# Optimization experiments

Measured on AMD Instinct MI355X. Metric: run time of the kernel, lower is better.

Reference implementation:

```python
import jax, jax.numpy as jnp
import numpy as np

B, S, H = 2, 1024, 4096
NH, NKV, D = 32, 8, 128
EPS = 1e-6
THETA = 10000.0


def rotate_half(x):
    x1, x2 = jnp.split(x, 2, axis=-1)
    return jnp.concatenate([-x2, x1], axis=-1)


def rmsnorm(x, w, eps):
    # RMSNorm over the last (head_dim) axis
    var = jnp.mean(x * x, axis=-1, keepdims=True)
    return x * jax.lax.rsqrt(var + eps) * w


def setup_inputs() -> dict:
    key = jax.random.key(0)
    ks = jax.random.split(key, 6)
    hidden_states = jax.random.normal(ks[0], (B, S, H), dtype=jnp.float32)
    # scaled init so activations stay O(1)
    Wq = jax.random.normal(ks[1], (NH * D, H), dtype=jnp.float32) * (H ** -0.5)
    Wk = jax.random.normal(ks[2], (NKV * D, H), dtype=jnp.float32) * (H ** -0.5)
    Wv = jax.random.normal(ks[3], (NKV * D, H), dtype=jnp.float32) * (H ** -0.5)
    Wo = jax.random.normal(ks[4], (H, NH * D), dtype=jnp.float32) * ((NH * D) ** -0.5)
    q_norm_w = jnp.ones((D,), dtype=jnp.float32)
    k_norm_w = jnp.ones((D,), dtype=jnp.float32)
    # standard default RoPE cos/sin tables, broadcast to [B, S, D]
    pos = jnp.arange(S, dtype=jnp.float32)
    inv_freq = 1.0 / (THETA ** (jnp.arange(0, D, 2, dtype=jnp.float32) / D))
    freqs = pos[:, None] * inv_freq[None, :]            # [S, D/2]
    emb = jnp.concatenate([freqs, freqs], axis=-1)      # [S, D]
    cos = jnp.broadcast_to(jnp.cos(emb)[None], (B, S, D)).astype(jnp.float32)
    sin = jnp.broadcast_to(jnp.sin(emb)[None], (B, S, D)).astype(jnp.float32)
    return dict(hidden_states=hidden_states, cos=cos, sin=sin,
                Wq=Wq, Wk=Wk, Wv=Wv, Wo=Wo,
                q_norm_w=q_norm_w, k_norm_w=k_norm_w)


def reference(hidden_states, cos, sin, Wq, Wk, Wv, Wo, q_norm_w, k_norm_w):
    b, s, h = hidden_states.shape
    # fused QKV projections (MojoLinear: y = x @ W.T, no bias)
    q = (hidden_states @ Wq.T).reshape(b, s, NH, D)
    k = (hidden_states @ Wk.T).reshape(b, s, NKV, D)
    v = (hidden_states @ Wv.T).reshape(b, s, NKV, D)
    # per-head-dim RMSNorm on q and k, then [B, H, S, D] layout
    q = rmsnorm(q, q_norm_w, EPS).transpose(0, 2, 1, 3)   # [B, NH,  S, D]
    k = rmsnorm(k, k_norm_w, EPS).transpose(0, 2, 1, 3)   # [B, NKV, S, D]
    v = v.transpose(0, 2, 1, 3)                           # [B, NKV, S, D]
    # RoPE (rotate-half)
    c = cos[:, None, :, :]
    sn = sin[:, None, :, :]
    q = q * c + rotate_half(q) * sn
    k = k * c + rotate_half(k) * sn
    # GQA: expand KV heads to query heads
    groups = NH // NKV
    k = jnp.repeat(k, groups, axis=1)                     # [B, NH, S, D]
    v = jnp.repeat(v, groups, axis=1)
    # causal attention (prefill with empty paged cache == causal SDPA)
    scores = jnp.einsum('bhqd,bhkd->bhqk', q, k) * (D ** -0.5)
    causal = jnp.tril(jnp.ones((s, s), dtype=bool))
    scores = jnp.where(causal, scores, jnp.finfo(scores.dtype).min)
    probs = jax.nn.softmax(scores, axis=-1)
    out = jnp.einsum('bhqk,bhkd->bhqd', probs, v)         # [B, NH, S, D]
    out = out.transpose(0, 2, 1, 3).reshape(b, s, NH * D)
    return out @ Wo.T
```

## Files before the change

kernel.cpp:

```cpp
#include <hip/hip_runtime.h>


typedef float  f32x4   __attribute__((ext_vector_type(4)));
typedef float  f32x16  __attribute__((ext_vector_type(16)));
typedef __bf16 bf16x8  __attribute__((ext_vector_type(8)));
typedef unsigned short u16x8 __attribute__((ext_vector_type(8)));

__device__ __forceinline__ unsigned short f2b(float f) {
    union { float f; unsigned int u; } x;
    x.f = f;
    unsigned int u = x.u;
    unsigned int r = u + 0x7fffu + ((u >> 16) & 1u);
    return (unsigned short)(r >> 16);
}

__device__ __forceinline__ void async16(const unsigned short* g, unsigned short* l) {
    __builtin_amdgcn_global_load_lds(
        (const __attribute__((address_space(1))) void*)g,
        (__attribute__((address_space(3))) void*)l, 16, 0, 0);
}

__global__ __launch_bounds__(256) void cvt_all(const float* __restrict__ hsrc,
                                               const float* __restrict__ wq,
                                               const float* __restrict__ wk,
                                               const float* __restrict__ wv,
                                               const float* __restrict__ wo,
                                               unsigned short* __restrict__ hidb,
                                               unsigned short* __restrict__ wqkvb,
                                               unsigned short* __restrict__ wob) {
    int i = blockIdx.x * 256 + threadIdx.x;
    if (i >= 6291456) return;
    const float* s; unsigned short* d; int j;
    if (i < 1048576)      { s = hsrc; d = hidb;             j = i; }
    else if (i < 3145728) { s = wq;   d = wqkvb;            j = i - 1048576; }
    else if (i < 3670016) { s = wk;   d = wqkvb + 16777216; j = i - 3145728; }
    else if (i < 4194304) { s = wv;   d = wqkvb + 20971520; j = i - 3670016; }
    else                  { s = wo;   d = wob;              j = i - 4194304; }
    const float4* s4 = (const float4*)s + (size_t)j * 2;
    float4 a = s4[0], b = s4[1];
    u16x8 o;
    o[0] = f2b(a.x); o[1] = f2b(a.y); o[2] = f2b(a.z); o[3] = f2b(a.w);
    o[4] = f2b(b.x); o[5] = f2b(b.y); o[6] = f2b(b.z); o[7] = f2b(b.w);
    *((u16x8*)d + j) = o;
}

__global__ __launch_bounds__(512, 2) void gemm256_bt(const unsigned short* __restrict__ A,
                                                     const unsigned short* __restrict__ W,
                                                     float* __restrict__ C) {
    constexpr int K = 4096, N = 6144;
    __shared__ __align__(16) unsigned short Ab[3][256 * 64];
    __shared__ __align__(16) unsigned short Bb[2][192 * 64];

    const int tid  = threadIdx.x;
    const int wave = tid >> 6, lane = tid & 63;
    const int wm   = wave >> 2, wn = wave & 3;
    const int l15  = lane & 15, h = lane >> 4;
    const int cx0  = (h ^ (l15 & 7)) << 3;
    const int cx1  = cx0 ^ 32;
    const int stgrow = wave * 8 + (lane >> 3);
    const int stgcol = ((lane & 7) ^ (lane >> 3)) << 3;
    const int aRow0 = blockIdx.y * 256;
    const int bRow0 = blockIdx.x * 192;
    const int NT = K >> 6;

#define STAGE_A(t, s, bi) async16(A + (size_t)(aRow0 + (s)*64 + stgrow) * K + (t)*64 + stgcol, \
                                  &Ab[bi][(s)*4096 + wave*512])
#define STAGE_B(t, s, bi) async16(W + (size_t)(bRow0 + (s)*64 + stgrow) * K + (t)*64 + stgcol, \
                                  &Bb[bi][(s)*4096 + wave*512])
#define RD_AQ(dst, buf, q) do { \
    _Pragma("unroll") \
    for (int mi = 0; mi < 2; mi++) { \
        const unsigned short* ap_ = (buf) + (wm * 128 + (q) * 32 + mi * 16 + l15) * 64; \
        dst[mi][0] = *(const bf16x8*)(ap_ + cx0); \
        dst[mi][1] = *(const bf16x8*)(ap_ + cx1); \
    } } while (0)
#define RD_B(dst, buf) do { \
    _Pragma("unroll") \
    for (int nf = 0; nf < 3; nf++) { \
        const unsigned short* bp_ = (buf) + (wn * 48 + nf * 16 + l15) * 64; \
        dst[nf][0] = *(const bf16x8*)(bp_ + cx0); \
        dst[nf][1] = *(const bf16x8*)(bp_ + cx1); \
    } } while (0)
#define MFMA_Q(q, AR, BR) do { \
    _Pragma("unroll") \
    for (int mi = 0; mi < 2; mi++) \
    _Pragma("unroll") \
    for (int nf = 0; nf < 3; nf++) { \
        acc[(q)*2+mi][nf] = __builtin_amdgcn_mfma_f32_16x16x32_bf16(AR[mi][0], BR[nf][0], acc[(q)*2+mi][nf], 0, 0, 0); \
        acc[(q)*2+mi][nf] = __builtin_amdgcn_mfma_f32_16x16x32_bf16(AR[mi][1], BR[nf][1], acc[(q)*2+mi][nf], 0, 0, 0); \
    } } while (0)
#define SB()      __builtin_amdgcn_sched_barrier(0)
#define BARRIER() __builtin_amdgcn_s_barrier()
#define PRIO1()   __builtin_amdgcn_s_setprio(1)
#define PRIO0()   __builtin_amdgcn_s_setprio(0)
#define LGKM(n)   asm volatile("s_waitcnt lgkmcnt(" #n ")" ::: "memory")

#define TILE(T, BC, BN_) do { \
    const int t_ = (T); \
    const unsigned short* Ab_ = Ab[t_ % 3]; \
    const int rb1 = (t_ & 1) ^ 1, ra2 = (t_ + 2) % 3; \
    const bool sb = (t_ + 1 < NT), sa = (t_ + 2 < NT); \
     \
    RD_AQ(rB, Ab_, 1); \
    if (sb) { STAGE_B(t_ + 1, 0, rb1); STAGE_B(t_ + 1, 1, rb1); STAGE_B(t_ + 1, 2, rb1); } \
    SB(); LGKM(4); SB(); \
    PRIO1(); MFMA_Q(0, rA, BC); PRIO0(); SB(); \
     \
    RD_AQ(rC, Ab_, 2); \
    if (sa) { STAGE_A(t_ + 2, 0, ra2); STAGE_A(t_ + 2, 1, ra2); } \
    SB(); LGKM(4); SB(); \
    PRIO1(); MFMA_Q(1, rB, BC); PRIO0(); SB(); \
     \
    RD_AQ(rD, Ab_, 3); \
    if (sa) { STAGE_A(t_ + 2, 2, ra2); STAGE_A(t_ + 2, 3, ra2); } \
    SB(); LGKM(4); SB(); \
    PRIO1(); MFMA_Q(2, rC, BC); PRIO0(); SB(); \
     \
    if (sa) asm volatile("s_waitcnt vmcnt(4)" ::: "memory"); \
    else    asm volatile("s_waitcnt vmcnt(0)" ::: "memory"); \
    SB(); BARRIER(); SB(); \
    if (sb) { RD_B(BN_, Bb[(t_ + 1) & 1]); RD_AQ(rA, Ab[(t_ + 1) % 3], 0); } \
    SB(); \
    if (sb) { LGKM(10); } else { LGKM(0); } \
    SB(); \
    PRIO1(); MFMA_Q(3, rD, BC); PRIO0(); SB(); \
} while (0)

    f32x4 acc[8][3] = {};
    bf16x8 rA[2][2], rB[2][2], rC[2][2], rD[2][2];
    bf16x8 bc[3][2], bn[3][2];

    STAGE_B(0, 0, 0); STAGE_B(0, 1, 0); STAGE_B(0, 2, 0);
    STAGE_A(0, 0, 0); STAGE_A(0, 1, 0); STAGE_A(0, 2, 0); STAGE_A(0, 3, 0);
    STAGE_A(1, 0, 1); STAGE_A(1, 1, 1); STAGE_A(1, 2, 1); STAGE_A(1, 3, 1);
    asm volatile("s_waitcnt vmcnt(4)" ::: "memory");
    SB(); BARRIER(); SB();
    RD_B(bc, Bb[0]);
    RD_AQ(rA, Ab[0], 0);
    SB();

    for (int t = 0; t < NT; t += 2) {
        TILE(t,     bc, bn);
        TILE(t + 1, bn, bc);
    }

    #pragma unroll
    for (int mf = 0; mf < 8; mf++)
        #pragma unroll
        for (int nf = 0; nf < 3; nf++)
            #pragma unroll
            for (int r = 0; r < 4; r++) {
                int row = aRow0 + wm * 128 + mf * 16 + h * 4 + r;
                int col = bRow0 + wn * 48 + nf * 16 + l15;
                C[(size_t)row * N + col] = acc[mf][nf][r];
            }
#undef STAGE_A
#undef STAGE_B
#undef RD_AQ
#undef RD_B
#undef MFMA_Q
#undef SB
#undef BARRIER
#undef PRIO1
#undef PRIO0
#undef LGKM
#undef TILE
}

__global__ __launch_bounds__(256) void gemm_bt_bf16(const unsigned short* __restrict__ A,
                                                    const unsigned short* __restrict__ W,
                                                    float* __restrict__ C,
                                                    int K, int N) {
    __shared__ __align__(16) unsigned short As[128 * 64];
    __shared__ __align__(16) unsigned short Bs[128 * 64];

    const int tid  = threadIdx.x;
    const int wave = tid >> 6, lane = tid & 63;
    const int wm   = wave >> 1, wn = wave & 1;
    const int l31  = lane & 31, lh = lane >> 5;
    const int arow = blockIdx.y * 128, brow = blockIdx.x * 128;

    int rr[4], gc[4], slot[4];
    #pragma unroll
    for (int it = 0; it < 4; it++) {
        slot[it] = it * 4 + wave;
        int ci = slot[it] * 64 + lane;
        rr[it] = ci >> 3;
        int c  = ci & 7;
        gc[it] = c ^ (rr[it] & 7);
    }

    f32x16 acc[2][2] = {};

    for (int k0 = 0; k0 < K; k0 += 64) {
        #pragma unroll
        for (int it = 0; it < 4; it++) {
            async16(A + (size_t)(arow + rr[it]) * K + k0 + gc[it] * 8, &As[slot[it] * 512]);
            async16(W + (size_t)(brow + rr[it]) * K + k0 + gc[it] * 8, &Bs[slot[it] * 512]);
        }
        __syncthreads();

        bf16x8 af[4][2], bfr[4][2];
        #pragma unroll
        for (int ks = 0; ks < 4; ks++) {
            #pragma unroll
            for (int i = 0; i < 2; i++) {
                int rowa = wm * 64 + i * 32 + l31;
                int ch   = (ks * 2 + lh) ^ (rowa & 7);
                af[ks][i]  = *(const bf16x8*)&As[rowa * 64 + ch * 8];
                int rowb = wn * 64 + i * 32 + l31;
                int chb  = (ks * 2 + lh) ^ (rowb & 7);
                bfr[ks][i] = *(const bf16x8*)&Bs[rowb * 64 + chb * 8];
            }
        }
        #pragma unroll
        for (int ks = 0; ks < 4; ks++)
            #pragma unroll
            for (int i = 0; i < 2; i++)
                #pragma unroll
                for (int j = 0; j < 2; j++)
                    acc[i][j] = __builtin_amdgcn_mfma_f32_32x32x16_bf16(af[ks][i], bfr[ks][j], acc[i][j], 0, 0, 0);
        __syncthreads();
    }

    #pragma unroll
    for (int i = 0; i < 2; i++)
        #pragma unroll
        for (int j = 0; j < 2; j++)
            #pragma unroll
            for (int r = 0; r < 16; r++) {
                int row = arow + wm * 64 + i * 32 + lh * 4 + (r & 3) + 8 * (r >> 2);
                int col = brow + wn * 64 + j * 32 + l31;
                C[(size_t)row * N + col] = acc[i][j][r];
            }
}

__global__ __launch_bounds__(256) void norm_rope(const float* __restrict__ X, int rstride,
                                                 const float* __restrict__ cosp,
                                                 const float* __restrict__ sinp,
                                                 const float* __restrict__ w,
                                                 unsigned short* __restrict__ Y, int nh) {
    const int wid  = blockIdx.x * 4 + (threadIdx.x >> 6);
    const int lane = threadIdx.x & 63;
    const int row  = wid / nh;
    const int h    = wid - row * nh;

    const float* xp = X + (size_t)row * rstride + h * 128;
    float x0 = xp[lane], x1 = xp[lane + 64];
    float ss = x0 * x0 + x1 * x1;
    #pragma unroll
    for (int off = 32; off; off >>= 1) ss += __shfl_xor(ss, off, 64);
    float r = rsqrtf(ss * (1.0f / 128.0f) + 1e-6f);
    float n0 = x0 * r * w[lane];
    float n1 = x1 * r * w[lane + 64];
    const float* cp = cosp + (size_t)row * 128;
    const float* sp = sinp + (size_t)row * 128;
    float y0 = n0 * cp[lane]      - n1 * sp[lane];
    float y1 = n1 * cp[lane + 64] + n0 * sp[lane + 64];
    const int b = row >> 10, s = row & 1023;
    unsigned short* yp = Y + (((size_t)(b * nh + h)) * 1024 + s) * 128;
    yp[lane]      = f2b(y0);
    yp[lane + 64] = f2b(y1);
}

__global__ __launch_bounds__(256) void v_trans(const float* __restrict__ V,
                                               unsigned short* __restrict__ Vt) {
    __shared__ float T[64][65];
    const int tid = threadIdx.x;
    const int st = blockIdx.x >> 1, dt = blockIdx.x & 1;
    const int bh = blockIdx.y, b = bh >> 3, h = bh & 7;

    const int sl = tid >> 2, c0 = (tid & 3) * 16;
    const float* src = V + (size_t)(b * 1024 + st * 64 + sl) * 6144 + h * 128 + dt * 64 + c0;
    #pragma unroll
    for (int j = 0; j < 4; j++) {
        float4 v = *(const float4*)(src + j * 4);
        *(float4*)&T[sl][c0 + j * 4] = v;
    }
    __syncthreads();

    const int dgrp = tid >> 6, sl2 = tid & 63;
    unsigned short* dst = Vt + (size_t)bh * 131072 + st * 64 + sl2;
    #pragma unroll
    for (int jd = 0; jd < 16; jd++) {
        int dl = dgrp * 16 + jd;
        dst[(size_t)(dt * 64 + dl) * 1024] = f2b(T[sl2][dl]);
    }
}

__global__ __launch_bounds__(256) void attn(const unsigned short* __restrict__ Qb,
                                            const unsigned short* __restrict__ Kb,
                                            const unsigned short* __restrict__ Vt,
                                            unsigned short* __restrict__ Ob) {
    __shared__ __align__(16) unsigned short Klds[128 * 128];
    __shared__ __align__(16) unsigned short Plds[4][16][136];

    const int tid  = threadIdx.x;
    const int w    = tid >> 6, lane = tid & 63;
    const int quad = lane >> 4, l15 = lane & 15;
    const int h = blockIdx.y, b = blockIdx.z, kvh = h >> 2;

    const unsigned short* Qp = Qb + ((size_t)(b * 32 + h))   * 131072;
    const unsigned short* Kp = Kb + ((size_t)(b * 8 + kvh))  * 131072;
    const unsigned short* Vp = Vt + ((size_t)(b * 8 + kvh))  * 131072;
    const float c2 = (float)(0.08838834764831845 * 1.4426950408889634);

    for (int half = 0; half < 2; half++) {
        const int qt = half ? (15 - (int)blockIdx.x) : (int)blockIdx.x;
        const int q0 = qt * 64;
        const int qrow = q0 + w * 16 + l15;

        bf16x8 qf[4];
        #pragma unroll
        for (int ks = 0; ks < 4; ks++)
            qf[ks] = *(const bf16x8*)(Qp + (size_t)qrow * 128 + ks * 32 + quad * 8);

        float m_i[4], l_i[4];
        #pragma unroll
        for (int r = 0; r < 4; r++) { m_i[r] = -1e30f; l_i[r] = 0.0f; }
        f32x4 o[8] = {};

        const int ntiles = (qt >> 1) + 1;
        const int nfull  = (qt * 64 + 1) >> 7;

        for (int kt = 0; kt < ntiles; kt++) {
            __syncthreads();
            #pragma unroll
            for (int it = 0; it < 8; it++) {
                int slot = it * 4 + w;
                int ci = slot * 64 + lane;
                int r = ci >> 4, c = ci & 15;
                int g = (c & 8) | ((c ^ r) & 7);
                async16(Kp + (size_t)(kt * 128 + r) * 128 + g * 8, &Klds[slot * 512]);
            }
            __syncthreads();

            f32x4 sacc[8] = {};
            __builtin_amdgcn_s_setprio(1);
            #pragma unroll
            for (int ks = 0; ks < 4; ks++) {
                #pragma unroll
                for (int tn = 0; tn < 8; tn++) {
                    int row = tn * 16 + l15;
                    int ch  = ks * 4 + quad;
                    int chs = (ch & 8) | ((ch ^ row) & 7);
                    bf16x8 kf = *(const bf16x8*)&Klds[row * 128 + chs * 8];
                    sacc[tn] = __builtin_amdgcn_mfma_f32_16x16x32_bf16(qf[ks], kf, sacc[tn], 0, 0, 0);
                }
            }
            __builtin_amdgcn_s_setprio(0);

            const bool masked = (kt >= nfull);
            #pragma unroll
            for (int r = 0; r < 4; r++) {
                float sv[8];
                float rmax = -1e30f;
                if (masked) {
                    const int qg = q0 + w * 16 + quad * 4 + r;
                    #pragma unroll
                    for (int tn = 0; tn < 8; tn++) {
                        float v = sacc[tn][r];
                        int kg = kt * 128 + tn * 16 + l15;
                        if (kg > qg) v = -1e30f;
                        sv[tn] = v;
                        rmax = fmaxf(rmax, v);
                    }
                } else {
                    #pragma unroll
                    for (int tn = 0; tn < 8; tn++) {
                        sv[tn] = sacc[tn][r];
                        rmax = fmaxf(rmax, sv[tn]);
                    }
                }
                #pragma unroll
                for (int off = 8; off; off >>= 1) rmax = fmaxf(rmax, __shfl_xor(rmax, off, 16));
                float mnew  = fmaxf(m_i[r], rmax);
                float alpha = __builtin_amdgcn_exp2f((m_i[r] - mnew) * c2);
                float rsum  = 0.0f;
                #pragma unroll
                for (int tn = 0; tn < 8; tn++) {
                    float p = __builtin_amdgcn_exp2f((sv[tn] - mnew) * c2);
                    sv[tn] = p;
                    rsum += p;
                }
                #pragma unroll
                for (int off = 8; off; off >>= 1) rsum += __shfl_xor(rsum, off, 16);
                m_i[r] = mnew;
                l_i[r] = l_i[r] * alpha + rsum;
                #pragma unroll
                for (int td = 0; td < 8; td++) o[td][r] *= alpha;
                #pragma unroll
                for (int tn = 0; tn < 8; tn++)
                    Plds[w][quad * 4 + r][tn * 16 + l15] = f2b(sv[tn]);
            }

            __builtin_amdgcn_s_setprio(1);
            #pragma unroll
            for (int ks = 0; ks < 4; ks++) {
                bf16x8 pf = *(const bf16x8*)&Plds[w][l15][ks * 32 + quad * 8];
                #pragma unroll
                for (int td = 0; td < 8; td++) {
                    bf16x8 vf = *(const bf16x8*)(Vp + (size_t)(td * 16 + l15) * 1024 + kt * 128 + ks * 32 + quad * 8);
                    o[td] = __builtin_amdgcn_mfma_f32_16x16x32_bf16(pf, vf, o[td], 0, 0, 0);
                }
            }
            __builtin_amdgcn_s_setprio(0);
        }

        #pragma unroll
        for (int r = 0; r < 4; r++) {
            float inv = 1.0f / l_i[r];
            const int qg = q0 + w * 16 + quad * 4 + r;
            unsigned short* op = Ob + ((size_t)(b * 1024 + qg)) * 4096 + h * 128;
            #pragma unroll
            for (int td = 0; td < 8; td++)
                op[td * 16 + l15] = f2b(o[td][r] * inv);
        }
    }
}

extern "C" void kernel_launch(void* const* d_in, const int* in_sizes, int n_in,
                              void* d_out, int out_size, void* d_ws, size_t ws_size,
                              hipStream_t stream) {
    const float* hid  = (const float*)d_in[0];
    const float* cosp = (const float*)d_in[1];
    const float* sinp = (const float*)d_in[2];
    const float* Wq   = (const float*)d_in[3];
    const float* Wk   = (const float*)d_in[4];
    const float* Wv   = (const float*)d_in[5];
    const float* Wo   = (const float*)d_in[6];
    const float* qw   = (const float*)d_in[7];
    const float* kw   = (const float*)d_in[8];
    float* out = (float*)d_out;

    char* ws = (char*)d_ws;
    float* QKVf = (float*)ws;
    unsigned short* Ob = (unsigned short*)ws;
    size_t off = (size_t)2048 * 6144 * 4;
    unsigned short* hidb  = (unsigned short*)(ws + off); off += (size_t)2048 * 4096 * 2;
    unsigned short* Wqkvb = (unsigned short*)(ws + off); off += (size_t)6144 * 4096 * 2;
    unsigned short* Wob   = (unsigned short*)(ws + off);
    unsigned short* Qb    = hidb;
    unsigned short* Kb    = Wqkvb;
    unsigned short* Vt    = Wqkvb + (size_t)2048 * 1024;

    dim3 blk(256);
    cvt_all<<<24576, blk, 0, stream>>>(hid, Wq, Wk, Wv, Wo, hidb, Wqkvb, Wob);
    gemm256_bt<<<dim3(32, 8), dim3(512), 0, stream>>>(hidb, Wqkvb, QKVf);
    norm_rope<<<16384, blk, 0, stream>>>(QKVf,        6144, cosp, sinp, qw, Qb, 32);
    norm_rope<<<4096,  blk, 0, stream>>>(QKVf + 4096, 6144, cosp, sinp, kw, Kb, 8);
    v_trans<<<dim3(32, 16), blk, 0, stream>>>(QKVf + 5120, Vt);
    attn<<<dim3(8, 32, 2), blk, 0, stream>>>(Qb, Kb, Vt, Ob);
    gemm_bt_bf16<<<dim3(32, 16), blk, 0, stream>>>(Ob, Wob, out, 4096, 4096);
}
```

Before: 503.8 us.

## Prefetch next K tile into registers in attention and merge Q/K norm-rope launches

The attention kernel replaces the synchronous global-to-LDS async K load with a register prefetch: the next K tile is loaded into registers during the QK^T and softmax of the current tile, then written to LDS after a barrier, so memory latency overlaps compute. Separately, the two norm_rope launches for Q and K are merged into a single launch that branches on warp index. The register staging raises VGPR pressure and adds an extra barrier per tile, which could reduce occupancy.

```diff
diff --git a/kernel.cpp b/kernel.cpp
--- a/kernel.cpp
+++ b/kernel.cpp
@@ -235,30 +235,33 @@
             }
 }
 
-__global__ __launch_bounds__(256) void norm_rope(const float* __restrict__ X, int rstride,
-                                                 const float* __restrict__ cosp,
-                                                 const float* __restrict__ sinp,
-                                                 const float* __restrict__ w,
-                                                 unsigned short* __restrict__ Y, int nh) {
+__global__ __launch_bounds__(256) void norm_rope2(const float* __restrict__ X,
+                                                  const float* __restrict__ cosp,
+                                                  const float* __restrict__ sinp,
+                                                  const float* __restrict__ qw,
+                                                  const float* __restrict__ kw,
+                                                  unsigned short* __restrict__ Qb,
+                                                  unsigned short* __restrict__ Kb) {
     const int wid  = blockIdx.x * 4 + (threadIdx.x >> 6);
     const int lane = threadIdx.x & 63;
-    const int row  = wid / nh;
-    const int h    = wid - row * nh;
-
-    const float* xp = X + (size_t)row * rstride + h * 128;
+    int row, hh, nh; const float* xb; const float* wv; unsigned short* Y;
+    if (wid < 65536) { row = wid >> 5; hh = wid & 31; nh = 32; xb = X;        wv = qw; Y = Qb; }
+    else { int w2 = wid - 65536; row = w2 >> 3; hh = w2 & 7; nh = 8; xb = X + 4096; wv = kw; Y = Kb; }
+
+    const float* xp = xb + (size_t)row * 6144 + hh * 128;
     float x0 = xp[lane], x1 = xp[lane + 64];
     float ss = x0 * x0 + x1 * x1;
     #pragma unroll
     for (int off = 32; off; off >>= 1) ss += __shfl_xor(ss, off, 64);
     float r = rsqrtf(ss * (1.0f / 128.0f) + 1e-6f);
-    float n0 = x0 * r * w[lane];
-    float n1 = x1 * r * w[lane + 64];
+    float n0 = x0 * r * wv[lane];
+    float n1 = x1 * r * wv[lane + 64];
     const float* cp = cosp + (size_t)row * 128;
     const float* sp = sinp + (size_t)row * 128;
     float y0 = n0 * cp[lane]      - n1 * sp[lane];
     float y1 = n1 * cp[lane + 64] + n0 * sp[lane + 64];
     const int b = row >> 10, s = row & 1023;
-    unsigned short* yp = Y + (((size_t)(b * nh + h)) * 1024 + s) * 128;
+    unsigned short* yp = Y + (((size_t)(b * nh + hh)) * 1024 + s) * 128;
     yp[lane]      = f2b(y0);
     yp[lane + 64] = f2b(y1);
 }
@@ -305,6 +308,22 @@
     const unsigned short* Vp = Vt + ((size_t)(b * 8 + kvh))  * 131072;
     const float c2 = (float)(0.08838834764831845 * 1.4426950408889634);
 
+    int boff[8], loff[8];
+    #pragma unroll
+    for (int it = 0; it < 8; it++) {
+        int slot = it * 4 + w;
+        int ci = slot * 64 + lane;
+        int r = ci >> 4, c = ci & 15;
+        int g = (c & 8) | ((c ^ r) & 7);
+        boff[it] = r * 128 + g * 8;
+        loff[it] = slot * 512 + lane * 8;
+    }
+    uint4 kreg[8];
+#define KLOAD(kt) do { _Pragma("unroll") for (int it = 0; it < 8; it++) \
+        kreg[it] = *(const uint4*)(Kp + (size_t)(kt) * 16384 + boff[it]); } while (0)
+#define KWRITE() do { _Pragma("unroll") for (int it = 0; it < 8; it++) \
+        *(uint4*)&Klds[loff[it]] = kreg[it]; } while (0)
+
     for (int half = 0; half < 2; half++) {
         const int qt = half ? (15 - (int)blockIdx.x) : (int)blockIdx.x;
         const int q0 = qt * 64;
@@ -323,17 +342,12 @@
         const int ntiles = (qt >> 1) + 1;
         const int nfull  = (qt * 64 + 1) >> 7;
 
+        KLOAD(0);
+        KWRITE();
+        __syncthreads();
+
         for (int kt = 0; kt < ntiles; kt++) {
-            __syncthreads();
-            #pragma unroll
-            for (int it = 0; it < 8; it++) {
-                int slot = it * 4 + w;
-                int ci = slot * 64 + lane;
-                int r = ci >> 4, c = ci & 15;
-                int g = (c & 8) | ((c ^ r) & 7);
-                async16(Kp + (size_t)(kt * 128 + r) * 128 + g * 8, &Klds[slot * 512]);
-            }
-            __syncthreads();
+            if (kt + 1 < ntiles) KLOAD(kt + 1);
 
             f32x4 sacc[8] = {};
             __builtin_amdgcn_s_setprio(1);
@@ -394,6 +408,9 @@
                     Plds[w][quad * 4 + r][tn * 16 + l15] = f2b(sv[tn]);
             }
 
+            __syncthreads();
+            if (kt + 1 < ntiles) KWRITE();
+
             __builtin_amdgcn_s_setprio(1);
             #pragma unroll
             for (int ks = 0; ks < 4; ks++) {
@@ -405,6 +422,7 @@
                 }
             }
             __builtin_amdgcn_s_setprio(0);
+            __syncthreads();
         }
 
         #pragma unroll
@@ -417,6 +435,8 @@
                 op[td * 16 + l15] = f2b(o[td][r] * inv);
         }
     }
+#undef KLOAD
+#undef KWRITE
 }
 
 extern "C" void kernel_launch(void* const* d_in, const int* in_sizes, int n_in,
@@ -447,8 +467,7 @@
     dim3 blk(256);
     cvt_all<<<24576, blk, 0, stream>>>(hid, Wq, Wk, Wv, Wo, hidb, Wqkvb, Wob);
     gemm256_bt<<<dim3(32, 8), dim3(512), 0, stream>>>(hidb, Wqkvb, QKVf);
-    norm_rope<<<16384, blk, 0, stream>>>(QKVf,        6144, cosp, sinp, qw, Qb, 32);
-    norm_rope<<<4096,  blk, 0, stream>>>(QKVf + 4096, 6144, cosp, sinp, kw, Kb, 8);
+    norm_rope2<<<20480, blk, 0, stream>>>(QKVf, cosp, sinp, qw, kw, Qb, Kb);
     v_trans<<<dim3(32, 16), blk, 0, stream>>>(QKVf + 5120, Vt);
     attn<<<dim3(8, 32, 2), blk, 0, stream>>>(Qb, Kb, Vt, Ob);
     gemm_bt_bf16<<<dim3(32, 16), blk, 0, stream>>>(Ob, Wob, out, 4096, 4096);
```

After: 520.6 us. +3.3%, slower.
